# Kernel tuning notes

Measured on AMD Instinct MI355X. Metric: run time of the kernel, lower is better.

Reference implementation:

```python
import jax, jax.numpy as jnp
import numpy as np

B, L, H, Di, N, K, R = 2, 512, 2048, 4096, 16, 4, 128


def setup_inputs() -> dict:
    key = jax.random.key(0)
    ks = jax.random.split(key, 8)
    s = 0.02
    inp = {
        "x": jax.random.normal(ks[0], (B, L, H), jnp.float32),
        "in_w": jax.random.normal(ks[1], (2 * Di, H), jnp.float32) * s,
        "in_b": jnp.zeros((2 * Di,), jnp.float32),
        "conv_w": jax.random.normal(ks[2], (Di, 1, K), jnp.float32) * s,  # depthwise conv weight
        "conv_b": jnp.zeros((Di,), jnp.float32),
        "xproj_w": jax.random.normal(ks[3], (R + 2 * N, Di), jnp.float32) * s,
        "dt_w": jax.random.normal(ks[4], (Di, R), jnp.float32) * s,
        "dt_b": jax.random.normal(ks[5], (Di,), jnp.float32) * 0.1,
        "A_log": jnp.log(jnp.broadcast_to(jnp.arange(1, N + 1, dtype=jnp.float32)[None, :], (Di, N))) + jnp.zeros((Di, N), jnp.float32),
        "D": jnp.ones((Di,), jnp.float32),
        "out_w": jax.random.normal(ks[6], (H, Di), jnp.float32) * s,
        "out_b": jnp.zeros((H,), jnp.float32),
    }
    return inp


def reference(x, in_w, in_b, conv_w, conv_b, xproj_w, dt_w, dt_b, A_log, D, out_w, out_b):
    silu = jax.nn.silu
    # in_proj -> split into hidden path and gate
    proj = x @ in_w.T + in_b                       # [B, L, 2*Di]
    h, gate = jnp.split(proj, 2, axis=-1)          # each [B, L, Di]
    # causal depthwise conv1d over time
    hc = jnp.transpose(h, (0, 2, 1))               # [B, Di, L]
    hc = jax.lax.conv_general_dilated(
        hc, conv_w, window_strides=(1,), padding=[(K - 1, 0)],
        dimension_numbers=("NCH", "OIH", "NCH"), feature_group_count=Di)
    hc = silu(hc + conv_b[None, :, None])          # [B, Di, L]
    hs = jnp.transpose(hc, (0, 2, 1))              # [B, L, Di]
    # input-dependent SSM parameters
    sp = hs @ xproj_w.T                            # [B, L, R + 2N]
    ts, Bm, Cm = sp[..., :R], sp[..., R:R + N], sp[..., R + N:]
    dt = jax.nn.softplus(ts @ dt_w.T + dt_b)       # [B, L, Di]
    A = -jnp.exp(A_log)                            # [Di, N]
    dA = jnp.exp(dt[..., None] * A[None, None])    # [B, L, Di, N]
    dBu = dt[..., None] * Bm[:, :, None, :] * hs[..., None]  # [B, L, Di, N]

    # selective scan: s_t = dA_t * s_{t-1} + dBu_t ; y_t = s_t . C_t
    def step(s, inputs):
        dA_t, dBu_t, C_t = inputs                  # [B,Di,N], [B,Di,N], [B,N]
        s = dA_t * s + dBu_t
        y = jnp.einsum("bdn,bn->bd", s, C_t)
        return s, y

    s0 = jnp.zeros((x.shape[0], Di, N), x.dtype)
    _, ys = jax.lax.scan(step, s0, (jnp.swapaxes(dA, 0, 1), jnp.swapaxes(dBu, 0, 1), jnp.swapaxes(Cm, 0, 1)))
    y = jnp.transpose(ys, (1, 0, 2))               # [B, L, Di]
    y = (y + hs * D) * silu(gate)
    return y @ out_w.T + out_b                     # [B, L, H]
```

## Files before the change

### kernel.cpp

```cpp
#include <hip/hip_runtime.h>
#include <hip/hip_bf16.h>

typedef __hip_bfloat16 bf16;
typedef _Float16 fp16;
typedef short bf16x8 __attribute__((ext_vector_type(8)));
typedef float f32x4 __attribute__((ext_vector_type(4)));
typedef _Float16 half8 __attribute__((ext_vector_type(8)));

#define BB 2
#define LL 512
#define HH 2048
#define DI 4096
#define NST 16
#define KK 4
#define RR 128
#define BLM (BB*LL)
#define CN 16
#define LC (LL/CN)
#define ZXP 16
#define ZOUT 4
#define CONV_N (BLM*DI)
#define CVT4_N (HH*DI/4)

enum { MODE_PROJ = 0, MODE_XPROJ = 1, MODE_DT = 2, MODE_OUT = 3 };

__device__ __forceinline__ float sigmoidf_(float x) { return 1.f / (1.f + __expf(-x)); }
__device__ __forceinline__ float softplusf_(float x) {
    return fmaxf(x, 0.f) + log1pf(__expf(-fabsf(x)));
}
__device__ __forceinline__ unsigned int bfpack(float a, float b) {
    __hip_bfloat162 h = __float22bfloat162_rn(make_float2(a, b));
    union { __hip_bfloat162 h; unsigned int u; } cv; cv.h = h;
    return cv.u;
}

typedef const __attribute__((address_space(1))) unsigned int* gas_t;
typedef __attribute__((address_space(3))) unsigned int* las_t;
__device__ __forceinline__ void gld16(const void* g, void* l) {
    __builtin_amdgcn_global_load_lds((gas_t)g, (las_t)l, 16, 0, 0);
}

__device__ __forceinline__ void cvt_seg(const float* s, bf16* d, int i) {
    float4 v = ((const float4*)s)[i];
    uint2 o; o.x = bfpack(v.x, v.y); o.y = bfpack(v.z, v.w);
    ((uint2*)d)[i] = o;
}

__global__ __launch_bounds__(256) void cvt_all(
    const float* __restrict__ s0, bf16* __restrict__ d0, int n0,
    const float* __restrict__ s1, bf16* __restrict__ d1, int n1,
    const float* __restrict__ s2, bf16* __restrict__ d2, int n2,
    const float* __restrict__ s3, bf16* __restrict__ d3, int n3)
{
    int i = blockIdx.x * 256 + threadIdx.x;
    int stride = gridDim.x * 256;
    int t1 = n0 + n1, t2 = t1 + n2, t3 = t2 + n3;
    for (; i < t3; i += stride) {
        if      (i < n0) cvt_seg(s0, d0, i);
        else if (i < t1) cvt_seg(s1, d1, i - n0);
        else if (i < t2) cvt_seg(s2, d2, i - t1);
        else             cvt_seg(s3, d3, i - t2);
    }
}

template<int BM, int BN, int MODE>
__global__ __launch_bounds__(256) void gemm_bf16(
    const bf16* __restrict__ A, const bf16* __restrict__ Bw,
    int N, int K, int lda, int ldb,
    const float* __restrict__ bias,
    bf16* __restrict__ outh, bf16* __restrict__ outh2,
    fp16* __restrict__ s0, fp16* __restrict__ s1,
    fp16* __restrict__ s2, fp16* __restrict__ s3)
{
    __shared__ short sA[BM * 64];
    __shared__ short sB[BN * 64];
    const int tid = threadIdx.x;
    const int col0 = blockIdx.x * BN;
    const int row0 = blockIdx.y * BM;
    const int wave = tid >> 6;
    const int lane = tid & 63;
    constexpr int NJ = (BM == 64 || BN == 64) ? 2 : 4;
    const int wr = (BM == 128) ? ((wave >> 1) * 64) : 0;
    const int wc = (BM == 64) ? (wave * 32) : ((wave & 1) * (BN / 2));
    const int lr = lane & 15;
    const int q  = lane >> 4;
    const int sw = lane & 7;

    const int kpb = K / gridDim.z;
    const int kbeg = blockIdx.z * kpb;
    const int kend = kbeg + kpb;

    const int r0 = tid >> 3;
    const int kc  = (tid & 7) << 3;
    const int kcs = (((tid & 7) ^ ((tid >> 3) & 7)) << 3);

    f32x4 acc[4][NJ] = {};

    for (int k0 = kbeg; k0 < kend; k0 += 64) {
        #pragma unroll
        for (int p = 0; p < BM / 32; p++) {
            int r = r0 + p * 32;
            gld16(A + (size_t)(row0 + r) * lda + k0 + kcs, &sA[r * 64 + kc]);
        }
        #pragma unroll
        for (int p = 0; p < BN / 32; p++) {
            int rr = r0 + p * 32;
            int nb = col0 + rr; if (nb > N - 1) nb = N - 1;
            gld16(Bw + (size_t)nb * ldb + k0 + kcs, &sB[rr * 64 + kc]);
        }
        __syncthreads();
        bf16x8 af[2][4], bfr[2][NJ];
        #pragma unroll
        for (int kk = 0; kk < 2; kk++) {
            const int cs = ((kk * 4 + q) ^ sw) << 3;
            #pragma unroll
            for (int i = 0; i < 4; i++)
                af[kk][i] = *(const bf16x8*)(&sA[(wr + i * 16 + lr) * 64 + cs]);
            #pragma unroll
            for (int j = 0; j < NJ; j++)
                bfr[kk][j] = *(const bf16x8*)(&sB[(wc + j * 16 + lr) * 64 + cs]);
        }
        #pragma unroll
        for (int kk = 0; kk < 2; kk++)
            #pragma unroll
            for (int i = 0; i < 4; i++)
                #pragma unroll
                for (int j = 0; j < NJ; j++)
                    acc[i][j] = __builtin_amdgcn_mfma_f32_16x16x32_bf16(af[kk][i], bfr[kk][j], acc[i][j], 0, 0, 0);
        __syncthreads();
    }

    fp16* oslice = s0;
    if (MODE == MODE_OUT) {
        int z = blockIdx.z;
        oslice = (z == 0) ? s0 : (z == 1) ? s1 : (z == 2) ? s2 : s3;
    }
    const int drow = (lane >> 4) << 2;
    const int dcol = lane & 15;
    #pragma unroll
    for (int i = 0; i < 4; i++) {
        #pragma unroll
        for (int j = 0; j < NJ; j++) {
            int n = col0 + wc + j * 16 + dcol;
            if (n >= N) continue;
            float bv = bias ? bias[n] : 0.f;
            #pragma unroll
            for (int r = 0; r < 4; r++) {
                int m = row0 + wr + i * 16 + drow + r;
                float v = acc[i][j][r];
                if (MODE == MODE_PROJ) {
                    v += bv;
                    if (n < DI) outh2[(size_t)m * DI + n] = (bf16)v;
                    else        outh[(size_t)m * DI + (n - DI)] = (bf16)v;
                } else if (MODE == MODE_XPROJ) {
                    s0[(size_t)blockIdx.z * (BLM * 160) + (size_t)m * 160 + n] = (fp16)v;
                } else if (MODE == MODE_DT) {
                    s0[(size_t)m * DI + n] = (fp16)softplusf_(v + bv);
                } else {
                    oslice[(size_t)m * HH + n] = (fp16)v;
                }
            }
        }
    }
}

__global__ __launch_bounds__(256) void conv_cvtow(
    const bf16* __restrict__ h, const float* __restrict__ conv_w,
    const float* __restrict__ conv_b, bf16* __restrict__ hs_b,
    const float* __restrict__ ow, bf16* __restrict__ ow_b)
{
    int i = blockIdx.x * 256 + threadIdx.x;
    int stride = gridDim.x * 256;
    for (; i < CONV_N + CVT4_N; i += stride) {
        if (i < CONV_N) {
            int idx = i;
            int d = idx & (DI - 1);
            int l = (idx >> 12) & (LL - 1);
            float acc = conv_b[d];
            #pragma unroll
            for (int k = 0; k < KK; k++) {
                int ls = l - (KK - 1) + k;
                if (ls >= 0) acc += (float)h[(size_t)idx + (size_t)(ls - l) * DI] * conv_w[d * KK + k];
            }
            float s = acc * sigmoidf_(acc);
            hs_b[idx] = (bf16)s;
        } else {
            cvt_seg(ow, ow_b, i - CONV_N);
        }
    }
}

__global__ __launch_bounds__(256) void reduce_sp(
    const fp16* __restrict__ spS, float* __restrict__ sp_f, bf16* __restrict__ ts_b)
{
    int i = blockIdx.x * 256 + threadIdx.x;
    int row = i / 20, c8 = (i % 20) * 8;
    float r[8] = {};
    #pragma unroll
    for (int z = 0; z < ZXP; z++) {
        half8 v = *(const half8*)&spS[(size_t)z * (BLM * 160) + (size_t)row * 160 + c8];
        #pragma unroll
        for (int e = 0; e < 8; e++) r[e] += (float)v[e];
    }
    *(float4*)&sp_f[(size_t)row * 160 + c8]     = make_float4(r[0], r[1], r[2], r[3]);
    *(float4*)&sp_f[(size_t)row * 160 + c8 + 4] = make_float4(r[4], r[5], r[6], r[7]);
    if (c8 < RR) {
        uint4 o = make_uint4(bfpack(r[0], r[1]), bfpack(r[2], r[3]),
                             bfpack(r[4], r[5]), bfpack(r[6], r[7]));
        *(uint4*)&ts_b[(size_t)row * RR + c8] = o;
    }
}

__global__ __launch_bounds__(256) void reduce_out(
    const fp16* __restrict__ s0, const fp16* __restrict__ s1,
    const fp16* __restrict__ s2, const fp16* __restrict__ s3,
    const float* __restrict__ bias, float* __restrict__ out)
{
    int i = blockIdx.x * 256 + threadIdx.x;
    int c8 = (i & 255) << 3;
    half8 a = ((const half8*)s0)[i];
    half8 b = ((const half8*)s1)[i];
    half8 c = ((const half8*)s2)[i];
    half8 d = ((const half8*)s3)[i];
    float r[8];
    #pragma unroll
    for (int e = 0; e < 8; e++)
        r[e] = (float)a[e] + (float)b[e] + (float)c[e] + (float)d[e] + bias[c8 + e];
    ((float4*)out)[2 * i]     = make_float4(r[0], r[1], r[2], r[3]);
    ((float4*)out)[2 * i + 1] = make_float4(r[4], r[5], r[6], r[7]);
}

__global__ __launch_bounds__(256) void scan_part1(
    const fp16* __restrict__ dtr, const float* __restrict__ sp,
    const bf16* __restrict__ hs_b, const float* __restrict__ A_log,
    float* __restrict__ P_ws, float* __restrict__ S_ws)
{
    int bid = blockIdx.x;
    int c  = bid & (CN - 1);
    int db = (bid >> 4) & (DI / 256 - 1);
    int b  = bid >> 8;
    int d  = db * 256 + threadIdx.x;

    float A[NST], P[NST], S[NST];
    #pragma unroll
    for (int n = 0; n < NST; n++) {
        A[n] = -__expf(A_log[d * NST + n]);
        P[n] = 1.f; S[n] = 0.f;
    }
    const float* spb = sp + (size_t)b * LL * 160;
    size_t base = (size_t)b * LL * DI + d;
    for (int l = c * LC; l < (c + 1) * LC; l++) {
        size_t off = base + (size_t)l * DI;
        float dtv = (float)dtr[off];
        float hsv = (float)hs_b[off];
        float dh = dtv * hsv;
        #pragma unroll
        for (int n = 0; n < NST; n++) {
            float a  = __expf(dtv * A[n]);
            float Bn = spb[l * 160 + RR + n];
            S[n] = a * S[n] + dh * Bn;
            P[n] *= a;
        }
    }
    size_t ob = (size_t)(b * CN + c) * NST * DI + d;
    #pragma unroll
    for (int n = 0; n < NST; n++) {
        P_ws[ob + (size_t)n * DI] = P[n];
        S_ws[ob + (size_t)n * DI] = S[n];
    }
}

__global__ __launch_bounds__(256) void scan_part2(
    const fp16* __restrict__ dtr, const float* __restrict__ sp,
    const bf16* __restrict__ hs_b, const bf16* __restrict__ g_b,
    const float* __restrict__ A_log, const float* __restrict__ Dv,
    const float* __restrict__ P_ws, const float* __restrict__ S_ws,
    bf16* __restrict__ y_b)
{
    int bid = blockIdx.x;
    int c  = bid & (CN - 1);
    int db = (bid >> 4) & (DI / 256 - 1);
    int b  = bid >> 8;
    int d  = db * 256 + threadIdx.x;

    float s[NST];
    #pragma unroll
    for (int n = 0; n < NST; n++) s[n] = 0.f;
    for (int j = 0; j < c; j++) {
        size_t ojb = (size_t)(b * CN + j) * NST * DI + d;
        #pragma unroll
        for (int n = 0; n < NST; n++)
            s[n] = P_ws[ojb + (size_t)n * DI] * s[n] + S_ws[ojb + (size_t)n * DI];
    }

    float A[NST];
    #pragma unroll
    for (int n = 0; n < NST; n++) A[n] = -__expf(A_log[d * NST + n]);
    float Dd = Dv[d];

    const float* spb = sp + (size_t)b * LL * 160;
    size_t base = (size_t)b * LL * DI + d;
    for (int l = c * LC; l < (c + 1) * LC; l++) {
        size_t off = base + (size_t)l * DI;
        float dtv = (float)dtr[off];
        float hsv = (float)hs_b[off];
        float dh = dtv * hsv;
        float y = 0.f;
        #pragma unroll
        for (int n = 0; n < NST; n++) {
            float a  = __expf(dtv * A[n]);
            float Bn = spb[l * 160 + RR + n];
            float Cn = spb[l * 160 + RR + NST + n];
            s[n] = a * s[n] + dh * Bn;
            y += s[n] * Cn;
        }
        float gv = (float)g_b[off];
        y_b[off] = (bf16)((y + hsv * Dd) * (gv * sigmoidf_(gv)));
    }
}

extern "C" void kernel_launch(void* const* d_in, const int* in_sizes, int n_in,
                              void* d_out, int out_size, void* d_ws, size_t ws_size,
                              hipStream_t stream)
{
    const float* x       = (const float*)d_in[0];
    const float* in_w    = (const float*)d_in[1];
    const float* in_b    = (const float*)d_in[2];
    const float* conv_w  = (const float*)d_in[3];
    const float* conv_b  = (const float*)d_in[4];
    const float* xproj_w = (const float*)d_in[5];
    const float* dt_w    = (const float*)d_in[6];
    const float* dt_b    = (const float*)d_in[7];
    const float* A_log   = (const float*)d_in[8];
    const float* Dv      = (const float*)d_in[9];
    const float* out_w   = (const float*)d_in[10];
    const float* out_b   = (const float*)d_in[11];
    float* out = (float*)d_out;

    char* ws = (char*)d_ws;
    const size_t MB = 1u << 20;
    bf16*  h_b    = (bf16*)(ws);
    fp16*  spS    = (fp16*)(ws);
    float* P_ws   = (float*)(ws);
    fp16*  oS0    = (fp16*)(ws);
    fp16*  oS1    = (fp16*)(ws + 4 * MB);
    bf16*  x_b    = (bf16*)(ws + 8 * MB);
    float* S_ws   = (float*)(ws + 8 * MB);
    fp16*  oS2    = (fp16*)(ws + 8 * MB);
    fp16*  oS3    = (fp16*)(ws + 12 * MB);
    bf16*  in_w_b = (bf16*)(ws + 16 * MB);
    bf16*  ow_b   = (bf16*)(ws + 16 * MB);
    bf16*  y_b    = (bf16*)(ws + 32 * MB);
    fp16*  dt_h   = (fp16*)(ws + 40 * MB);
    bf16*  hs_b   = (bf16*)(ws + 48 * MB);
    bf16*  g_b    = (bf16*)(ws + 56 * MB);
    char* p = ws + 64 * MB;
    float* sp_f = (float*)p; p += (size_t)BLM * 160 * 4;
    bf16*  ts_b = (bf16*)p;  p += (size_t)BLM * RR * 2;
    bf16*  xw_b = (bf16*)p;  p += (size_t)(RR + 2 * NST) * DI * 2;
    bf16*  dtw_b= (bf16*)p;  p += (size_t)DI * RR * 2;

    cvt_all<<<2048, 256, 0, stream>>>(
        x, x_b, BLM * HH / 4,
        in_w, in_w_b, 2 * DI * HH / 4,
        xproj_w, xw_b, (RR + 2 * NST) * DI / 4,
        dt_w, dtw_b, DI * RR / 4);
    gemm_bf16<128, 64, MODE_PROJ><<<dim3((2 * DI) / 64, BLM / 128, 1), 256, 0, stream>>>(
        x_b, in_w_b, 2 * DI, HH, HH, HH, in_b, g_b, h_b,
        nullptr, nullptr, nullptr, nullptr);
    conv_cvtow<<<2048, 256, 0, stream>>>(h_b, conv_w, conv_b, hs_b, out_w, ow_b);
    gemm_bf16<64, 128, MODE_XPROJ><<<dim3(2, BLM / 64, ZXP), 256, 0, stream>>>(
        hs_b, xw_b, RR + 2 * NST, DI, DI, DI, nullptr, nullptr, nullptr,
        spS, nullptr, nullptr, nullptr);
    reduce_sp<<<80, 256, 0, stream>>>(spS, sp_f, ts_b);
    gemm_bf16<64, 128, MODE_DT><<<dim3(DI / 128, BLM / 64, 1), 256, 0, stream>>>(
        ts_b, dtw_b, DI, RR, RR, RR, dt_b, nullptr, nullptr,
        dt_h, nullptr, nullptr, nullptr);
    scan_part1<<<BB * (DI / 256) * CN, 256, 0, stream>>>(
        dt_h, sp_f, hs_b, A_log, P_ws, S_ws);
    scan_part2<<<BB * (DI / 256) * CN, 256, 0, stream>>>(
        dt_h, sp_f, hs_b, g_b, A_log, Dv, P_ws, S_ws, y_b);
    gemm_bf16<128, 64, MODE_OUT><<<dim3(HH / 64, BLM / 128, ZOUT), 256, 0, stream>>>(
        y_b, ow_b, HH, DI, DI, DI, nullptr, nullptr, nullptr,
        oS0, oS1, oS2, oS3);
    reduce_out<<<1024, 256, 0, stream>>>(oS0, oS1, oS2, oS3, out_b, out);
}
```

Before: 351.1 us.

## Split scan state across 4 lanes and add separate chunk-prefix kernel

Each scan thread now handles 4 of the 16 SSM states for one channel instead of all 16. Four lanes combine their partial outputs with shuffles, which gives four times as many blocks and fewer registers per thread. The serial carry over chunks that each part2 block used to redo is moved into a new scan_mid kernel, which writes per-chunk initial states in place. The cost is an extra kernel launch, redundant loads of dt/hs across the 4 lanes, and a write from only 1 lane in 4.

Measured after the change: 343.4 us. -2.2%, faster.

```diff
diff --git a/kernel.cpp b/kernel.cpp
--- a/kernel.cpp
+++ b/kernel.cpp
@@ -237,15 +237,17 @@
 {
     int bid = blockIdx.x;
     int c  = bid & (CN - 1);
-    int db = (bid >> 4) & (DI / 256 - 1);
-    int b  = bid >> 8;
-    int d  = db * 256 + threadIdx.x;
-
-    float A[NST], P[NST], S[NST];
-    #pragma unroll
-    for (int n = 0; n < NST; n++) {
-        A[n] = -__expf(A_log[d * NST + n]);
-        P[n] = 1.f; S[n] = 0.f;
+    int db = (bid >> 4) & 63;
+    int b  = bid >> 10;
+    int ng = threadIdx.x & 3;
+    int d  = db * 64 + (threadIdx.x >> 2);
+    int n0 = ng * 4;
+
+    float A[4], P[4], S[4];
+    #pragma unroll
+    for (int k = 0; k < 4; k++) {
+        A[k] = -__expf(A_log[d * NST + n0 + k]);
+        P[k] = 1.f; S[k] = 0.f;
     }
     const float* spb = sp + (size_t)b * LL * 160;
     size_t base = (size_t)b * LL * DI + d;
@@ -255,18 +257,37 @@
         float hsv = (float)hs_b[off];
         float dh = dtv * hsv;
         #pragma unroll
-        for (int n = 0; n < NST; n++) {
-            float a  = __expf(dtv * A[n]);
-            float Bn = spb[l * 160 + RR + n];
-            S[n] = a * S[n] + dh * Bn;
-            P[n] *= a;
-        }
-    }
-    size_t ob = (size_t)(b * CN + c) * NST * DI + d;
-    #pragma unroll
-    for (int n = 0; n < NST; n++) {
-        P_ws[ob + (size_t)n * DI] = P[n];
-        S_ws[ob + (size_t)n * DI] = S[n];
+        for (int k = 0; k < 4; k++) {
+            float a  = __expf(dtv * A[k]);
+            float Bn = spb[l * 160 + RR + n0 + k];
+            S[k] = a * S[k] + dh * Bn;
+            P[k] *= a;
+        }
+    }
+    size_t ob = (size_t)(b * CN + c) * NST * DI + (size_t)n0 * DI + d;
+    #pragma unroll
+    for (int k = 0; k < 4; k++) {
+        P_ws[ob + (size_t)k * DI] = P[k];
+        S_ws[ob + (size_t)k * DI] = S[k];
+    }
+}
+
+__global__ __launch_bounds__(256) void scan_mid(
+    const float* __restrict__ P_ws, float* __restrict__ S_ws)
+{
+    int bid = blockIdx.x;
+    int n  = bid & (NST - 1);
+    int db = (bid >> 4) & (DI / 256 - 1);
+    int b  = bid >> 8;
+    int d  = db * 256 + threadIdx.x;
+    size_t base = (size_t)n * DI + d;
+    float s = 0.f;
+    for (int c = 0; c < CN; c++) {
+        size_t idx = (size_t)(b * CN + c) * NST * DI + base;
+        float p  = P_ws[idx];
+        float sv = S_ws[idx];
+        S_ws[idx] = s;
+        s = p * s + sv;
     }
 }
 
@@ -274,28 +295,23 @@
     const fp16* __restrict__ dtr, const float* __restrict__ sp,
     const bf16* __restrict__ hs_b, const bf16* __restrict__ g_b,
     const float* __restrict__ A_log, const float* __restrict__ Dv,
-    const float* __restrict__ P_ws, const float* __restrict__ S_ws,
-    bf16* __restrict__ y_b)
+    const float* __restrict__ I_ws, bf16* __restrict__ y_b)
 {
     int bid = blockIdx.x;
     int c  = bid & (CN - 1);
-    int db = (bid >> 4) & (DI / 256 - 1);
-    int b  = bid >> 8;
-    int d  = db * 256 + threadIdx.x;
-
-    float s[NST];
-    #pragma unroll
-    for (int n = 0; n < NST; n++) s[n] = 0.f;
-    for (int j = 0; j < c; j++) {
-        size_t ojb = (size_t)(b * CN + j) * NST * DI + d;
-        #pragma unroll
-        for (int n = 0; n < NST; n++)
-            s[n] = P_ws[ojb + (size_t)n * DI] * s[n] + S_ws[ojb + (size_t)n * DI];
-    }
-
-    float A[NST];
-    #pragma unroll
-    for (int n = 0; n < NST; n++) A[n] = -__expf(A_log[d * NST + n]);
+    int db = (bid >> 4) & 63;
+    int b  = bid >> 10;
+    int ng = threadIdx.x & 3;
+    int d  = db * 64 + (threadIdx.x >> 2);
+    int n0 = ng * 4;
+
+    float A[4], s[4];
+    #pragma unroll
+    for (int k = 0; k < 4; k++)
+        A[k] = -__expf(A_log[d * NST + n0 + k]);
+    size_t ib = (size_t)(b * CN + c) * NST * DI + (size_t)n0 * DI + d;
+    #pragma unroll
+    for (int k = 0; k < 4; k++) s[k] = I_ws[ib + (size_t)k * DI];
     float Dd = Dv[d];
 
     const float* spb = sp + (size_t)b * LL * 160;
@@ -307,15 +323,19 @@
         float dh = dtv * hsv;
         float y = 0.f;
         #pragma unroll
-        for (int n = 0; n < NST; n++) {
-            float a  = __expf(dtv * A[n]);
-            float Bn = spb[l * 160 + RR + n];
-            float Cn = spb[l * 160 + RR + NST + n];
-            s[n] = a * s[n] + dh * Bn;
-            y += s[n] * Cn;
-        }
-        float gv = (float)g_b[off];
-        y_b[off] = (bf16)((y + hsv * Dd) * (gv * sigmoidf_(gv)));
+        for (int k = 0; k < 4; k++) {
+            float a  = __expf(dtv * A[k]);
+            float Bn = spb[l * 160 + RR + n0 + k];
+            float Cn = spb[l * 160 + RR + NST + n0 + k];
+            s[k] = a * s[k] + dh * Bn;
+            y += s[k] * Cn;
+        }
+        y += __shfl_xor(y, 1);
+        y += __shfl_xor(y, 2);
+        if (ng == 0) {
+            float gv = (float)g_b[off];
+            y_b[off] = (bf16)((y + hsv * Dd) * (gv * sigmoidf_(gv)));
+        }
     }
 }
 
@@ -376,10 +396,11 @@
     gemm_bf16<64, 128, MODE_DT><<<dim3(DI / 128, BLM / 64, 1), 256, 0, stream>>>(
         ts_b, dtw_b, DI, RR, RR, RR, dt_b, nullptr, nullptr,
         dt_h, nullptr, nullptr, nullptr);
-    scan_part1<<<BB * (DI / 256) * CN, 256, 0, stream>>>(
+    scan_part1<<<BB * (DI / 64) * CN, 256, 0, stream>>>(
         dt_h, sp_f, hs_b, A_log, P_ws, S_ws);
-    scan_part2<<<BB * (DI / 256) * CN, 256, 0, stream>>>(
-        dt_h, sp_f, hs_b, g_b, A_log, Dv, P_ws, S_ws, y_b);
+    scan_mid<<<BB * NST * (DI / 256), 256, 0, stream>>>(P_ws, S_ws);
+    scan_part2<<<BB * (DI / 64) * CN, 256, 0, stream>>>(
+        dt_h, sp_f, hs_b, g_b, A_log, Dv, S_ws, y_b);
     gemm_bf16<128, 64, MODE_OUT><<<dim3(HH / 64, BLM / 128, ZOUT), 256, 0, stream>>>(
         y_b, ow_b, HH, DI, DI, DI, nullptr, nullptr, nullptr,
         oS0, oS1, oS2, oS3);
```
